# Optimization experiments

Measured on AMD Instinct MI355X. Metric: run time of the kernel, lower is better.

## Reference

```python
import jax, jax.numpy as jnp
import numpy as np

IN_SHAPE = (128, 128, 128)   # (d, w, h)
RES_SCALE = 1.5
SCAN_RANGE = 11.0
PROJ_NUM = 4
SPACING = np.array([1.0, 1.0, 1.0])
OUT_SHAPE = (256, 256)
BATCH = 2


def _make_grids():
    # Faithful numpy port of proj_layer._project_grid_multi (precomputed buffers).
    d, w, h = IN_SHAPE
    p = PROJ_NUM
    half = SCAN_RANGE / 2.0
    poses = np.zeros((p, 3))
    poses[:, 1] = 3.0
    poses[:, 0] = np.tan(np.linspace(-half, half, p) / 180.0 * np.pi) * 3.0
    poses[:, 2] = np.linspace(-0.2, 0.2, p)
    emi = poses * w                                  # emitter positions, (p,3)
    res_d, res_h = int(d * RES_SCALE), int(h * RES_SCALE)
    Nvec = np.array([0.0, 1.0, 0.0])
    P0 = np.linspace(0, w - 1, w)[:, None] * np.array([[0.0, 1.0, 0.0]])  # (w,3)
    lin_x = np.linspace(-res_d / 2, res_d / 2 - 1, res_d)
    lin_y = np.linspace(-res_h / 2, res_h / 2 - 1, res_h)
    gx, gy = np.meshgrid(lin_x, lin_y, indexing='ij')
    I = np.stack([gx, np.zeros_like(gx), gy], axis=-1)   # (rd,rh,3) detector plane
    I = I[None] - emi[:, None, None, :]                  # (p,rd,rh,3) ray dirs
    dxr = I / I[..., 1:2]
    In = I / np.linalg.norm(I, axis=3, keepdims=True)
    dxr = np.linalg.norm(dxr * SPACING[None, None, None, :], axis=3)  # (p,rd,rh) step length
    inv_IN = 1.0 / (In @ Nvec)                           # (p,rd,rh)
    PN = (P0[None] - emi[:, None, :]) @ Nvec             # (p,w)
    T = inv_IN[..., None] * PN[:, None, None, :]         # (p,rd,rh,w) ray params
    grid = In[..., None, :] * T[..., None] + emi[:, None, None, None, :]  # (p,rd,rh,w,3)
    gn = np.empty_like(grid)
    gn[..., 0] = grid[..., 0] / d * 2.0
    gn[..., 1] = grid[..., 1] / w * 2.0 - 1.0
    gn[..., 2] = grid[..., 2] / h * 2.0
    gn = gn[..., ::-1]  # torch.flip(grid, [4]) -> grid_sample (x,y,z) order
    return np.ascontiguousarray(gn).astype(np.float32), dxr.astype(np.float32)


def setup_inputs() -> dict:
    key = jax.random.key(0)
    x = jax.random.normal(key, (BATCH,) + IN_SHAPE, dtype=jnp.float32)
    g, dxr = _make_grids()
    return {"x": x, "grids": jnp.asarray(g), "dx": jnp.asarray(dxr)}


def _trilinear_gather(vol, coords):
    # vol: (b, D, H, W); coords: (N,3) normalized [-1,1], (x,y,z) -> (W,H,D)
    # F.grid_sample(mode='bilinear', padding_mode='zeros', align_corners=True)
    b, D, H, W = vol.shape
    ix = (coords[:, 0] + 1.0) * 0.5 * (W - 1)
    iy = (coords[:, 1] + 1.0) * 0.5 * (H - 1)
    iz = (coords[:, 2] + 1.0) * 0.5 * (D - 1)
    x0, y0, z0 = jnp.floor(ix), jnp.floor(iy), jnp.floor(iz)
    fx, fy, fz = ix - x0, iy - y0, iz - z0
    volf = vol.reshape(b, -1)
    out = jnp.zeros((b, coords.shape[0]), vol.dtype)
    for dz in (0, 1):
        wz = fz if dz else 1.0 - fz
        zi = z0 + dz
        for dy in (0, 1):
            wy = fy if dy else 1.0 - fy
            yi = y0 + dy
            for dxx in (0, 1):
                wx = fx if dxx else 1.0 - fx
                xi = x0 + dxx
                valid = ((xi >= 0) & (xi <= W - 1) & (yi >= 0) & (yi <= H - 1)
                         & (zi >= 0) & (zi <= D - 1))
                idx = ((jnp.clip(zi, 0, D - 1).astype(jnp.int32) * H
                        + jnp.clip(yi, 0, H - 1).astype(jnp.int32)) * W
                       + jnp.clip(xi, 0, W - 1).astype(jnp.int32))
                wgt = jnp.where(valid, wx * wy * wz, 0.0)
                out = out + volf[:, idx] * wgt[None, :]
    return out


def _nearest_resize(t, out_hw):
    # F.interpolate(mode='nearest'): src = floor(dst * in / out)
    b, c, H, W = t.shape
    oh, ow = out_hw
    hi = jnp.minimum((jnp.arange(oh) * H) // oh, H - 1)
    wi = jnp.minimum((jnp.arange(ow) * W) // ow, W - 1)
    return t[:, :, hi][:, :, :, wi]


def reference(x, grids, dx):
    p, rd, rh, w = grids.shape[:4]
    b = x.shape[0]
    coords = grids.reshape(-1, 3)                       # (p*rd*rh*w, 3)
    samples = _trilinear_gather(x, coords).reshape(b, p, rd, rh, w)
    x_proj = samples.sum(axis=4) * dx[None]             # ray-sum projection
    return _nearest_resize(x_proj, OUT_SHAPE)
```

## Files before the change

kernel.cpp:

```cpp
#include <hip/hip_runtime.h>

#define DD   128
#define HH   128
#define WW   128
#define PNUM 4
#define RD   192
#define RH   192
#define OHH  256
#define OWW  256
#define NB   2
#define ROWS (PNUM * RD * RH)
#define VOL  (DD * HH * WW)
#define WSPL 8

typedef float vf4 __attribute__((ext_vector_type(4)));


__global__ __launch_bounds__(256) void ray_setup_kernel(
    const float* __restrict__ grids,
    float* __restrict__ rayp)
{
    const int ray = (int)(blockIdx.x * 256 + threadIdx.x);
    const float* g = grids + (size_t)ray * 384;
    const vf4 L0 = *(const vf4*)g;
    const vf4 L1 = *(const vf4*)(g + 192);
    vf4 r;
    r.x = (L0.x + 1.f) * 63.5f;
    r.y = (L1.x - L0.x) * 0.9921875f;
    r.z = (L0.z + 1.f) * 63.5f;
    r.w = (L1.z - L0.z) * 0.9921875f;
    *(vf4*)(rayp + (size_t)ray * 4) = r;
}

__global__ __launch_bounds__(256) void interleave_kernel(
    const float* __restrict__ x,
    float* __restrict__ vol4)
{
    const int i  = (int)(blockIdx.x * 256 + threadIdx.x);
    const int xc = i & 127;
    const float a0 = x[i];
    const float a1 = x[VOL + i];
    const float b0 = (xc < 127) ? x[i + 1]       : a0;
    const float b1 = (xc < 127) ? x[VOL + i + 1] : a1;
    vf4 q; q.x = a0; q.y = a1; q.z = b0; q.w = b1;
    *(vf4*)(vol4 + (size_t)i * 4) = q;
}

__global__ __launch_bounds__(256, 8) void proj_kernel(
    const float* __restrict__ vol4,
    const float* __restrict__ rayp,
    float* __restrict__ part)
{
    const int tid  = (int)(blockIdx.x * 256 + threadIdx.x);
    const int lane = tid & 63;
    const int wave = tid >> 6;
    const int wc   = wave & (WSPL - 1);
    const int ray  = (wave >> 3) * 64 + lane;

    const vf4 rp = *(const vf4*)(rayp + (size_t)ray * 4);
    const int wbase = wc * (WW / WSPL);

    float s0 = 0.f, s1 = 0.f;

#pragma unroll 2
    for (int wu = 0; wu < WW / WSPL; ++wu) {
        const int   w  = wbase + wu;
        const float wf = (float)w;
        const float ix = fmaf(wf, rp.y, rp.x);
        const float iz = fmaf(wf, rp.w, rp.z);

        const float WY0 = wf * 0.0078125f;
        const float WY1 = 1.f - WY0;
        const int   r0  = (w > 0) ? (w - 1) : 0;
        const int   r1  = w;

        const float xf = floorf(ix);
        const float fx = ix - xf;
        const int   xb = (int)xf;
        const int   xl = min(max(xb, 0), 126);
        const bool  inx = (xb >= 0) && (xb <= 126);
        const float WL = inx ? (1.f - fx) : ((xb == -1)  ? fx         : 0.f);
        const float WR = inx ? fx         : ((xb == 127) ? (1.f - fx) : 0.f);

        const float zf = floorf(iz);
        const float fz = iz - zf;
        const int   zb  = (int)zf;
        const int   zi0 = min(max(zb,     0), 127);
        const int   zi1 = min(max(zb + 1, 0), 127);
        const float WZ0 = (zb >= 0  && zb <= 127) ? (1.f - fz) : 0.f;
        const float WZ1 = (zb >= -1 && zb <= 126) ? fz         : 0.f;

        const int zo0 = zi0 << 14;
        const int zo1 = zi1 << 14;
        const int yo0 = r0 << 7;
        const int yo1 = r1 << 7;

        const vf4 q00 = *(const vf4*)(vol4 + (size_t)(zo0 + yo0 + xl) * 4);
        const vf4 q01 = *(const vf4*)(vol4 + (size_t)(zo0 + yo1 + xl) * 4);
        const vf4 q10 = *(const vf4*)(vol4 + (size_t)(zo1 + yo0 + xl) * 4);
        const vf4 q11 = *(const vf4*)(vol4 + (size_t)(zo1 + yo1 + xl) * 4);

        const float u00 = WZ0 * WY0, u01 = WZ0 * WY1;
        const float u10 = WZ1 * WY0, u11 = WZ1 * WY1;

        s0 = fmaf(u00, fmaf(WL, q00.x, WR * q00.z), s0);
        s1 = fmaf(u00, fmaf(WL, q00.y, WR * q00.w), s1);
        s0 = fmaf(u01, fmaf(WL, q01.x, WR * q01.z), s0);
        s1 = fmaf(u01, fmaf(WL, q01.y, WR * q01.w), s1);
        s0 = fmaf(u10, fmaf(WL, q10.x, WR * q10.z), s0);
        s1 = fmaf(u10, fmaf(WL, q10.y, WR * q10.w), s1);
        s0 = fmaf(u11, fmaf(WL, q11.x, WR * q11.z), s0);
        s1 = fmaf(u11, fmaf(WL, q11.y, WR * q11.w), s1);
    }

    part[((size_t)wc * NB + 0) * ROWS + ray] = s0;
    part[((size_t)wc * NB + 1) * ROWS + ray] = s1;
}


__global__ __launch_bounds__(256) void proj_rays_fb_kernel(
    const float* __restrict__ x,
    const float* __restrict__ grids,
    float* __restrict__ part)
{
    const int tid  = (int)(blockIdx.x * blockDim.x + threadIdx.x);
    const int wave = tid >> 6;
    const int lane = tid & 63;
    const int wcc  = wave & 3;
    const int rr   = wave >> 2;
    const int ray  = rr * 64 + lane;

    const float* g  = grids + (size_t)ray * 384 + wcc * 96;
    const float* v0 = x;
    const float* v1 = x + VOL;

    float s0 = 0.f, s1 = 0.f;
    for (int w0 = 0; w0 < 32; w0 += 16) {
        const vf4* gc = (const vf4*)(g + w0 * 3);
        float cf[48];
#pragma unroll
        for (int i = 0; i < 12; ++i) {
            const vf4 t = gc[i];
            cf[4*i+0] = t.x; cf[4*i+1] = t.y; cf[4*i+2] = t.z; cf[4*i+3] = t.w;
        }
#pragma unroll
        for (int w = 0; w < 16; ++w) {
            const float ix = (cf[3*w+0] + 1.f) * 63.5f;
            const float iy = (cf[3*w+1] + 1.f) * 63.5f;
            const float iz = (cf[3*w+2] + 1.f) * 63.5f;
            const float x0f = floorf(ix), y0f = floorf(iy), z0f = floorf(iz);
            const float fxx = ix - x0f, fyy = iy - y0f, fzz = iz - z0f;
            const float wx0 = (x0f >= 0.f && x0f <= 127.f) ? (1.f-fxx) : 0.f;
            const float wx1 = (x0f+1.f >= 0.f && x0f+1.f <= 127.f) ? fxx : 0.f;
            const float wy0 = (y0f >= 0.f && y0f <= 127.f) ? (1.f-fyy) : 0.f;
            const float wy1 = (y0f+1.f >= 0.f && y0f+1.f <= 127.f) ? fyy : 0.f;
            const float wz0 = (z0f >= 0.f && z0f <= 127.f) ? (1.f-fzz) : 0.f;
            const float wz1 = (z0f+1.f >= 0.f && z0f+1.f <= 127.f) ? fzz : 0.f;
            const int xi0 = (int)fminf(fmaxf(x0f,0.f),127.f);
            const int xi1 = (int)fminf(fmaxf(x0f+1.f,0.f),127.f);
            const int yi0 = (int)fminf(fmaxf(y0f,0.f),127.f);
            const int yi1 = (int)fminf(fmaxf(y0f+1.f,0.f),127.f);
            const int zi0 = (int)fminf(fmaxf(z0f,0.f),127.f);
            const int zi1 = (int)fminf(fmaxf(z0f+1.f,0.f),127.f);
            const int b00 = (zi0*HH+yi0)*WW, b01 = (zi0*HH+yi1)*WW;
            const int b10 = (zi1*HH+yi0)*WW, b11 = (zi1*HH+yi1)*WW;
            const float w000 = wz0*wy0*wx0, w001 = wz0*wy0*wx1;
            const float w010 = wz0*wy1*wx0, w011 = wz0*wy1*wx1;
            const float w100 = wz1*wy0*wx0, w101 = wz1*wy0*wx1;
            const float w110 = wz1*wy1*wx0, w111 = wz1*wy1*wx1;
            s0 += w000*v0[b00+xi0] + w001*v0[b00+xi1] + w010*v0[b01+xi0] + w011*v0[b01+xi1]
                + w100*v0[b10+xi0] + w101*v0[b10+xi1] + w110*v0[b11+xi0] + w111*v0[b11+xi1];
            s1 += w000*v1[b00+xi0] + w001*v1[b00+xi1] + w010*v1[b01+xi0] + w011*v1[b01+xi1]
                + w100*v1[b10+xi0] + w101*v1[b10+xi1] + w110*v1[b11+xi0] + w111*v1[b11+xi1];
        }
        g += 0;
    }
    part[((size_t)wcc * NB + 0) * ROWS + ray] = s0;
    part[((size_t)wcc * NB + 1) * ROWS + ray] = s1;
}


__global__ __launch_bounds__(256) void resize_reduce_kernel(
    const float* __restrict__ part,
    const float* __restrict__ dx,
    float* __restrict__ out,
    int wsplit)
{
    const int idx = (int)(blockIdx.x * blockDim.x + threadIdx.x);
    const int ow = idx & (OWW - 1);
    const int oh = (idx >> 8) & (OHH - 1);
    const int bp = idx >> 16;
    const int b  = bp >> 2;
    const int p  = bp & 3;
    const int hi = (oh * 3) >> 2;
    const int wi = (ow * 3) >> 2;
    const int ray = (p * RD + hi) * RH + wi;

    float s = 0.f;
    for (int wcc = 0; wcc < wsplit; ++wcc)
        s += part[((size_t)wcc * NB + b) * ROWS + ray];
    out[idx] = s * dx[ray];
}

extern "C" void kernel_launch(void* const* d_in, const int* in_sizes, int n_in,
                              void* d_out, int out_size, void* d_ws, size_t ws_size,
                              hipStream_t stream) {
    const float* x     = (const float*)d_in[0];
    const float* grids = (const float*)d_in[1];
    const float* dx    = (const float*)d_in[2];
    float* out = (float*)d_out;
    float* ws  = (float*)d_ws;

    const size_t NEED = (size_t)(VOL * 4 + ROWS * 4 + WSPL * NB * ROWS) * 4;

    if (ws_size >= NEED) {
        float* vol4 = ws;
        float* rayp = vol4 + (size_t)VOL * 4;
        float* part = rayp + (size_t)ROWS * 4;

        ray_setup_kernel <<<ROWS / 256, 256, 0, stream>>>(grids, rayp);
        interleave_kernel<<<VOL / 256, 256, 0, stream>>>(x, vol4);
        proj_kernel      <<<ROWS * WSPL / 256, 256, 0, stream>>>(vol4, rayp, part);
        resize_reduce_kernel<<<(NB * PNUM * OHH * OWW) / 256, 256, 0, stream>>>(part, dx, out, WSPL);
    } else {
        float* part = ws;
        proj_rays_fb_kernel<<<ROWS * 4 / 256, 256, 0, stream>>>(x, grids, part);
        resize_reduce_kernel<<<(NB * PNUM * OHH * OWW) / 256, 256, 0, stream>>>(part, dx, out, 4);
    }
}
```

Measured before the change: 336.3 us.

## Pre-blend y-interpolation into bf16 w-major volume, shrink per-sample gathers

Because the y weights depend only on the sample index w, the preprocessing kernel now folds the two-row y interpolation into a w-major precomputed volume. It stores both batches and both x neighbours packed as bf16 in 8 bytes per voxel. The projection kernel then does two 8-byte gathers per sample instead of four 16-byte ones. The per-ray z parameters are hoisted to once per detector row, and blocks are remapped so each block covers rays from the same row. This cuts memory traffic and ALU work in the hot loop, at the cost of bf16 rounding of the volume values, which may affect accuracy.

```diff
diff --git a/kernel.cpp b/kernel.cpp
--- a/kernel.cpp
+++ b/kernel.cpp
@@ -1,8 +1,6 @@
 #include <hip/hip_runtime.h>
-
-#define DD   128
-#define HH   128
-#define WW   128
+#include <hip/hip_bf16.h>
+
 #define PNUM 4
 #define RD   192
 #define RH   192
@@ -10,69 +8,104 @@
 #define OWW  256
 #define NB   2
 #define ROWS (PNUM * RD * RH)
-#define VOL  (DD * HH * WW)
+#define VOL  (128 * 128 * 128)
 #define WSPL 8
 
-typedef float vf4 __attribute__((ext_vector_type(4)));
+typedef float        vf4 __attribute__((ext_vector_type(4)));
+typedef float        vf2 __attribute__((ext_vector_type(2)));
+typedef unsigned int vu2 __attribute__((ext_vector_type(2)));
+
+__device__ __forceinline__ unsigned int bf16_bits(float f) {
+    __hip_bfloat16 h = __float2bfloat16(f);
+    return (unsigned int)__hip_bfloat16_raw(h).x;
+}
+__device__ __forceinline__ float hi_bits_f(unsigned int u) {
+    u &= 0xffff0000u;
+    return __builtin_bit_cast(float, u);
+}
+__device__ __forceinline__ float lo_bits_f(unsigned int u) {
+    u <<= 16;
+    return __builtin_bit_cast(float, u);
+}
 
 
 __global__ __launch_bounds__(256) void ray_setup_kernel(
     const float* __restrict__ grids,
-    float* __restrict__ rayp)
+    float* __restrict__ rayp,
+    float* __restrict__ zp)
 {
     const int ray = (int)(blockIdx.x * 256 + threadIdx.x);
     const float* g = grids + (size_t)ray * 384;
     const vf4 L0 = *(const vf4*)g;
     const vf4 L1 = *(const vf4*)(g + 192);
-    vf4 r;
+    vf2 r;
     r.x = (L0.x + 1.f) * 63.5f;
     r.y = (L1.x - L0.x) * 0.9921875f;
-    r.z = (L0.z + 1.f) * 63.5f;
-    r.w = (L1.z - L0.z) * 0.9921875f;
-    *(vf4*)(rayp + (size_t)ray * 4) = r;
-}
-
-__global__ __launch_bounds__(256) void interleave_kernel(
+    *(vf2*)(rayp + (size_t)ray * 2) = r;
+    if ((ray % RH) == 0) {
+        vf2 z;
+        z.x = (L0.z + 1.f) * 63.5f;
+        z.y = (L1.z - L0.z) * 0.9921875f;
+        *(vf2*)(zp + (size_t)(ray / RH) * 2) = z;
+    }
+}
+
+__global__ __launch_bounds__(256) void ycomb_kernel(
     const float* __restrict__ x,
-    float* __restrict__ vol4)
+    vu2* __restrict__ ycomb)
 {
     const int i  = (int)(blockIdx.x * 256 + threadIdx.x);
+    const int w  = i >> 14;
+    const int z  = (i >> 7) & 127;
     const int xc = i & 127;
-    const float a0 = x[i];
-    const float a1 = x[VOL + i];
-    const float b0 = (xc < 127) ? x[i + 1]       : a0;
-    const float b1 = (xc < 127) ? x[VOL + i + 1] : a1;
-    vf4 q; q.x = a0; q.y = a1; q.z = b0; q.w = b1;
-    *(vf4*)(vol4 + (size_t)i * 4) = q;
+
+    const float WY0 = (float)w * 0.0078125f;
+    const float WY1 = 1.f - WY0;
+    const int   rm  = (w > 0) ? (w - 1) : 0;
+
+    const int b0 = (z * 128 + rm) * 128;
+    const int b1 = (z * 128 + w) * 128;
+    const int x1 = (xc < 127) ? (xc + 1) : 127;
+
+    const float a0 = fmaf(WY0, x[b0 + xc],       WY1 * x[b1 + xc]);
+    const float a1 = fmaf(WY0, x[VOL + b0 + xc], WY1 * x[VOL + b1 + xc]);
+    const float c0 = fmaf(WY0, x[b0 + x1],       WY1 * x[b1 + x1]);
+    const float c1 = fmaf(WY0, x[VOL + b0 + x1], WY1 * x[VOL + b1 + x1]);
+
+    vu2 q;
+    q.x = bf16_bits(a0) | (bf16_bits(a1) << 16);
+    q.y = bf16_bits(c0) | (bf16_bits(c1) << 16);
+    ycomb[i] = q;
 }
 
 __global__ __launch_bounds__(256, 8) void proj_kernel(
-    const float* __restrict__ vol4,
+    const vu2*  __restrict__ ycomb,
     const float* __restrict__ rayp,
+    const float* __restrict__ zp,
     float* __restrict__ part)
 {
-    const int tid  = (int)(blockIdx.x * 256 + threadIdx.x);
-    const int lane = tid & 63;
-    const int wave = tid >> 6;
-    const int wc   = wave & (WSPL - 1);
-    const int ray  = (wave >> 3) * 64 + lane;
-
-    const vf4 rp = *(const vf4*)(rayp + (size_t)ray * 4);
-    const int wbase = wc * (WW / WSPL);
+    const int b    = (int)blockIdx.x;
+    const int rdp  = b / 6;
+    const int rem  = b % 6;
+    const int t    = rem >> 1;
+    const int h    = rem & 1;
+    const int wave = (int)threadIdx.x >> 6;
+    const int lane = (int)threadIdx.x & 63;
+    const int wc   = h * 4 + wave;
+    const int ray  = rdp * RH + t * 64 + lane;
+
+    const vf2 xp = *(const vf2*)(rayp + (size_t)ray * 2);
+    const vf2 zv = *(const vf2*)(zp + (size_t)rdp * 2);
 
     float s0 = 0.f, s1 = 0.f;
-
-#pragma unroll 2
-    for (int wu = 0; wu < WW / WSPL; ++wu) {
+    const int wbase = wc * 16;
+
+#pragma unroll 4
+    for (int wu = 0; wu < 16; ++wu) {
         const int   w  = wbase + wu;
         const float wf = (float)w;
-        const float ix = fmaf(wf, rp.y, rp.x);
-        const float iz = fmaf(wf, rp.w, rp.z);
-
-        const float WY0 = wf * 0.0078125f;
-        const float WY1 = 1.f - WY0;
-        const int   r0  = (w > 0) ? (w - 1) : 0;
-        const int   r1  = w;
+        const float ix = fmaf(wf, xp.y, xp.x);
+        const float iz = fmaf(wf, zv.y, zv.x);
 
         const float xf = floorf(ix);
         const float fx = ix - xf;
@@ -90,27 +123,17 @@
         const float WZ0 = (zb >= 0  && zb <= 127) ? (1.f - fz) : 0.f;
         const float WZ1 = (zb >= -1 && zb <= 126) ? fz         : 0.f;
 
-        const int zo0 = zi0 << 14;
-        const int zo1 = zi1 << 14;
-        const int yo0 = r0 << 7;
-        const int yo1 = r1 << 7;
-
-        const vf4 q00 = *(const vf4*)(vol4 + (size_t)(zo0 + yo0 + xl) * 4);
-        const vf4 q01 = *(const vf4*)(vol4 + (size_t)(zo0 + yo1 + xl) * 4);
-        const vf4 q10 = *(const vf4*)(vol4 + (size_t)(zo1 + yo0 + xl) * 4);
-        const vf4 q11 = *(const vf4*)(vol4 + (size_t)(zo1 + yo1 + xl) * 4);
-
-        const float u00 = WZ0 * WY0, u01 = WZ0 * WY1;
-        const float u10 = WZ1 * WY0, u11 = WZ1 * WY1;
-
-        s0 = fmaf(u00, fmaf(WL, q00.x, WR * q00.z), s0);
-        s1 = fmaf(u00, fmaf(WL, q00.y, WR * q00.w), s1);
-        s0 = fmaf(u01, fmaf(WL, q01.x, WR * q01.z), s0);
-        s1 = fmaf(u01, fmaf(WL, q01.y, WR * q01.w), s1);
-        s0 = fmaf(u10, fmaf(WL, q10.x, WR * q10.z), s0);
-        s1 = fmaf(u10, fmaf(WL, q10.y, WR * q10.w), s1);
-        s0 = fmaf(u11, fmaf(WL, q11.x, WR * q11.z), s0);
-        s1 = fmaf(u11, fmaf(WL, q11.y, WR * q11.w), s1);
+        const int base = w << 14;
+        const vu2 q0 = ycomb[base + (zi0 << 7) + xl];
+        const vu2 q1 = ycomb[base + (zi1 << 7) + xl];
+
+        const float v00 = fmaf(WL, lo_bits_f(q0.x), WR * lo_bits_f(q0.y));
+        const float v01 = fmaf(WL, hi_bits_f(q0.x), WR * hi_bits_f(q0.y));
+        const float v10 = fmaf(WL, lo_bits_f(q1.x), WR * lo_bits_f(q1.y));
+        const float v11 = fmaf(WL, hi_bits_f(q1.x), WR * hi_bits_f(q1.y));
+
+        s0 = fmaf(WZ0, v00, fmaf(WZ1, v10, s0));
+        s1 = fmaf(WZ0, v01, fmaf(WZ1, v11, s1));
     }
 
     part[((size_t)wc * NB + 0) * ROWS + ray] = s0;
@@ -162,8 +185,8 @@
             const int yi1 = (int)fminf(fmaxf(y0f+1.f,0.f),127.f);
             const int zi0 = (int)fminf(fmaxf(z0f,0.f),127.f);
             const int zi1 = (int)fminf(fmaxf(z0f+1.f,0.f),127.f);
-            const int b00 = (zi0*HH+yi0)*WW, b01 = (zi0*HH+yi1)*WW;
-            const int b10 = (zi1*HH+yi0)*WW, b11 = (zi1*HH+yi1)*WW;
+            const int b00 = (zi0*128+yi0)*128, b01 = (zi0*128+yi1)*128;
+            const int b10 = (zi1*128+yi0)*128, b11 = (zi1*128+yi1)*128;
             const float w000 = wz0*wy0*wx0, w001 = wz0*wy0*wx1;
             const float w010 = wz0*wy1*wx0, w011 = wz0*wy1*wx1;
             const float w100 = wz1*wy0*wx0, w101 = wz1*wy0*wx1;
@@ -173,7 +196,6 @@
             s1 += w000*v1[b00+xi0] + w001*v1[b00+xi1] + w010*v1[b01+xi0] + w011*v1[b01+xi1]
                 + w100*v1[b10+xi0] + w101*v1[b10+xi1] + w110*v1[b11+xi0] + w111*v1[b11+xi1];
         }
-        g += 0;
     }
     part[((size_t)wcc * NB + 0) * ROWS + ray] = s0;
     part[((size_t)wcc * NB + 1) * ROWS + ray] = s1;
@@ -209,21 +231,26 @@
     const float* grids = (const float*)d_in[1];
     const float* dx    = (const float*)d_in[2];
     float* out = (float*)d_out;
-    float* ws  = (float*)d_ws;
-
-    const size_t NEED = (size_t)(VOL * 4 + ROWS * 4 + WSPL * NB * ROWS) * 4;
+    char*  ws  = (char*)d_ws;
+
+    const size_t YC_B   = (size_t)VOL * 8;
+    const size_t RAYP_B = (size_t)ROWS * 2 * 4;
+    const size_t ZP_B   = (size_t)PNUM * RD * 2 * 4;
+    const size_t PART_B = (size_t)WSPL * NB * ROWS * 4;
+    const size_t NEED   = YC_B + RAYP_B + ZP_B + PART_B;
 
     if (ws_size >= NEED) {
-        float* vol4 = ws;
-        float* rayp = vol4 + (size_t)VOL * 4;
-        float* part = rayp + (size_t)ROWS * 4;
-
-        ray_setup_kernel <<<ROWS / 256, 256, 0, stream>>>(grids, rayp);
-        interleave_kernel<<<VOL / 256, 256, 0, stream>>>(x, vol4);
-        proj_kernel      <<<ROWS * WSPL / 256, 256, 0, stream>>>(vol4, rayp, part);
+        vu2*   ycomb = (vu2*)ws;
+        float* rayp  = (float*)(ws + YC_B);
+        float* zp    = (float*)(ws + YC_B + RAYP_B);
+        float* part  = (float*)(ws + YC_B + RAYP_B + ZP_B);
+
+        ray_setup_kernel<<<ROWS / 256, 256, 0, stream>>>(grids, rayp, zp);
+        ycomb_kernel    <<<VOL / 256, 256, 0, stream>>>(x, ycomb);
+        proj_kernel     <<<(PNUM * RD) * 3 * 2, 256, 0, stream>>>(ycomb, rayp, zp, part);
         resize_reduce_kernel<<<(NB * PNUM * OHH * OWW) / 256, 256, 0, stream>>>(part, dx, out, WSPL);
     } else {
-        float* part = ws;
+        float* part = (float*)ws;
         proj_rays_fb_kernel<<<ROWS * 4 / 256, 256, 0, stream>>>(x, grids, part);
         resize_reduce_kernel<<<(NB * PNUM * OHH * OWW) / 256, 256, 0, stream>>>(part, dx, out, 4);
     }
```

New measurement: 310.4 us. 1.08x faster.
